# Kernel tuning notes

Hardware: AMD Instinct MI355X
Metric: run time of the kernel (lower is better)

Reference implementation:

```python
import jax, jax.numpy as jnp
import numpy as np
import math

B, S, D, H = 2, 2048, 1024, 16
DK = D // H

def setup_inputs() -> dict:
    key = jax.random.key(0)
    ks = jax.random.split(key, 12)
    scale = 0.02
    return {
        "q": jax.random.normal(ks[0], (B, S, D), jnp.float32),
        "k": jax.random.normal(ks[1], (B, S, D), jnp.float32),
        "v": jax.random.normal(ks[2], (B, S, D), jnp.float32),
        "mask": jnp.ones((B, S), jnp.int32),
        "Wq": jax.random.normal(ks[3], (D, D), jnp.float32) * scale,
        "bq": jnp.zeros((D,), jnp.float32),
        "Wk": jax.random.normal(ks[4], (D, D), jnp.float32) * scale,
        "bk": jnp.zeros((D,), jnp.float32),
        "Wv": jax.random.normal(ks[5], (D, D), jnp.float32) * scale,
        "bv": jnp.zeros((D,), jnp.float32),
        "Wo": jax.random.normal(ks[6], (D, D), jnp.float32) * scale,
        "bo": jnp.zeros((D,), jnp.float32),
    }

def _split_heads(x):
    b, s, d = x.shape
    return x.reshape(b, s, H, DK).transpose(0, 2, 1, 3)  # [b,h,s,dk]

def reference(q, k, v, mask, Wq, bq, Wk, bk, Wv, bv, Wo, bo):
    Q = _split_heads(q @ Wq.T + bq)
    K = _split_heads(k @ Wk.T + bk)
    V = _split_heads(v @ Wv.T + bv)
    scores = jnp.einsum('bhqd,bhkd->bhqk', Q, K) / math.sqrt(DK)
    # mask dim==2 path: [b,s] -> [b,1,1,s]
    m = mask[:, None, None, :]
    scores = jnp.where(m == 0, jnp.float32(-1e9), scores)
    attn = jax.nn.softmax(scores, axis=-1)  # dropout is identity in eval
    out = jnp.einsum('bhqk,bhkd->bhqd', attn, V)
    out = out.transpose(0, 2, 1, 3).reshape(q.shape[0], q.shape[1], D)
    return out @ Wo.T + bo
```

## Files before the change

### kernel.cpp

```cpp
#include <hip/hip_runtime.h>
#include <math.h>

#define D_MODEL 1024
#define NHEAD   16
#define DKH     64
#define SEQ     2048
#define BATCH   2
#define TOK     (BATCH*SEQ)

typedef short s16x8 __attribute__((ext_vector_type(8)));
typedef float f32x4 __attribute__((ext_vector_type(4)));
typedef unsigned short ushort_t;

__device__ inline unsigned short f2bf(float f) {
    union { float f; unsigned u; } v; v.f = f;
    unsigned r = v.u + 0x7FFFu + ((v.u >> 16) & 1u);
    return (unsigned short)(r >> 16);
}
__device__ inline float bf2f(ushort_t h) {
    union { unsigned u; float f; } v; v.u = (unsigned)h << 16;
    return v.f;
}
__device__ inline unsigned cvt_pk_bf16(float a, float b) {
    unsigned r;
    asm("v_cvt_pk_bf16_f32 %0, %1, %2" : "=v"(r) : "v"(a), "v"(b));
    return r;
}
__device__ inline void gload16(const void* g, void* l) {
    __builtin_amdgcn_global_load_lds(
        (const __attribute__((address_space(1))) void*)g,
        (__attribute__((address_space(3))) void*)l, 16, 0, 0);
}

__global__ __launch_bounds__(256) void convert_all(
    const float* __restrict__ q, const float* __restrict__ k,
    const float* __restrict__ v,
    const float* __restrict__ Wq, const float* __restrict__ Wk,
    const float* __restrict__ Wv, const float* __restrict__ Wo,
    const int* __restrict__ mask,
    ushort_t* __restrict__ qb, ushort_t* __restrict__ kb,
    ushort_t* __restrict__ vb,
    ushort_t* __restrict__ Wqb, ushort_t* __restrict__ Wkb,
    ushort_t* __restrict__ Wvb, ushort_t* __restrict__ Wohi,
    ushort_t* __restrict__ Wolo, float* __restrict__ mb)
{
    const int ACT4 = TOK * D_MODEL / 4;
    const int W4   = D_MODEL * D_MODEL / 4;
    const int total = 3 * ACT4 + 4 * W4 + TOK / 4;
    for (int u = blockIdx.x * 256 + threadIdx.x; u < total; u += gridDim.x * 256) {
        if (u < 3 * ACT4) {
            int which = u / ACT4, off = u - which * ACT4;
            const float* src = which == 0 ? q : which == 1 ? k : v;
            ushort_t*    dst = which == 0 ? qb : which == 1 ? kb : vb;
            float4 f = ((const float4*)src)[off];
            uint2 o;
            o.x = cvt_pk_bf16(f.x, f.y);
            o.y = cvt_pk_bf16(f.z, f.w);
            ((uint2*)dst)[off] = o;
        } else if (u < 3 * ACT4 + 3 * W4) {
            int uu = u - 3 * ACT4;
            int which = uu / W4, off = uu - which * W4;
            const float* src = which == 0 ? Wq : which == 1 ? Wk : Wv;
            ushort_t*    dst = which == 0 ? Wqb : which == 1 ? Wkb : Wvb;
            float4 f = ((const float4*)src)[off];
            uint2 o;
            o.x = cvt_pk_bf16(f.x, f.y);
            o.y = cvt_pk_bf16(f.z, f.w);
            ((uint2*)dst)[off] = o;
        } else if (u < 3 * ACT4 + 4 * W4) {
            int off = u - (3 * ACT4 + 3 * W4);
            float4 f = ((const float4*)Wo)[off];
            ushort_t h0 = f2bf(f.x), h1 = f2bf(f.y), h2 = f2bf(f.z), h3 = f2bf(f.w);
            uint2 hw;
            hw.x = (unsigned)h0 | ((unsigned)h1 << 16);
            hw.y = (unsigned)h2 | ((unsigned)h3 << 16);
            ((uint2*)Wohi)[off] = hw;
            uint2 lw;
            lw.x = cvt_pk_bf16(f.x - bf2f(h0), f.y - bf2f(h1));
            lw.y = cvt_pk_bf16(f.z - bf2f(h2), f.w - bf2f(h3));
            ((uint2*)Wolo)[off] = lw;
        } else {
            int off = u - (3 * ACT4 + 4 * W4);
            int4 m = ((const int4*)mask)[off];
            float4 f;
            f.x = m.x ? 0.f : -1e9f;
            f.y = m.y ? 0.f : -1e9f;
            f.z = m.z ? 0.f : -1e9f;
            f.w = m.w ? 0.f : -1e9f;
            ((float4*)mb)[off] = f;
        }
    }
}

__global__ __launch_bounds__(256) void gemm_qkv(
    const ushort_t* __restrict__ qb, const ushort_t* __restrict__ kb,
    const ushort_t* __restrict__ vb,
    const ushort_t* __restrict__ Wqb, const ushort_t* __restrict__ Wkb,
    const ushort_t* __restrict__ Wvb,
    const float* __restrict__ bqp, const float* __restrict__ bkp,
    const float* __restrict__ bvp,
    ushort_t* __restrict__ Qb, ushort_t* __restrict__ Kb,
    ushort_t* __restrict__ Vtb)
{
    __shared__ __align__(16) char pool[64 * 136 * 2];
    ushort_t* As = (ushort_t*)pool;
    ushort_t* Ws = As + 128 * 32;

    const int z = blockIdx.z;
    const ushort_t* Ain  = z == 0 ? qb : z == 1 ? kb : vb;
    const ushort_t* Wptr = z == 0 ? Wqb : z == 1 ? Wkb : Wvb;
    const float*    bias = z == 0 ? bqp : z == 1 ? bkp : bvp;

    const int hwid = blockIdx.x + 8 * blockIdx.y;
    const int work = (hwid & 7) * 32 + (hwid >> 3);
    const int m0 = (work >> 3) * 128;
    const int n0 = (work & 7) * 128;

    const int t = threadIdx.x;
    const int w = t >> 6, lane = t & 63, l15 = lane & 15, l4 = lane >> 4;
    const int wr = w >> 1, wc = w & 1;

    f32x4 acc[4][4];
#pragma unroll
    for (int m = 0; m < 4; ++m)
#pragma unroll
        for (int n = 0; n < 4; ++n) acc[m][n] = (f32x4){0.f, 0.f, 0.f, 0.f};

    const ushort_t* Ag = Ain  + (size_t)(m0 + (t >> 2)) * D_MODEL + (t & 3) * 8;
    const ushort_t* Wg = Wptr + (size_t)(n0 + (t >> 2)) * D_MODEL + (t & 3) * 8;
    ushort_t* AsW = As + w * 512;
    ushort_t* WsW = Ws + w * 512;

    for (int k0 = 0; k0 < D_MODEL; k0 += 32) {
        __syncthreads();
        gload16(Ag + k0, AsW);
        gload16(Ag + (size_t)64 * D_MODEL + k0, AsW + 2048);
        gload16(Wg + k0, WsW);
        gload16(Wg + (size_t)64 * D_MODEL + k0, WsW + 2048);
        __syncthreads();

        s16x8 af[4], bfr[4];
#pragma unroll
        for (int m = 0; m < 4; ++m)
            af[m] = *(const s16x8*)&As[(wr * 64 + m * 16 + l15) * 32 + l4 * 8];
#pragma unroll
        for (int n = 0; n < 4; ++n)
            bfr[n] = *(const s16x8*)&Ws[(wc * 64 + n * 16 + l15) * 32 + l4 * 8];
#pragma unroll
        for (int m = 0; m < 4; ++m)
#pragma unroll
            for (int n = 0; n < 4; ++n)
                acc[m][n] = __builtin_amdgcn_mfma_f32_16x16x32_bf16(af[m], bfr[n], acc[m][n], 0, 0, 0);
    }

    if (z == 2) {
        ushort_t* Ct = (ushort_t*)pool;
        const int h0 = n0 >> 6;
        const int bb = m0 >> 11;
        const int s0 = m0 & (SEQ - 1);
#pragma unroll
        for (int hh = 0; hh < 2; ++hh) {
            __syncthreads();
            if (wc == hh) {
#pragma unroll
                for (int n = 0; n < 4; ++n) {
                    const int nl = n * 16 + l15;
                    const float bv = bias[n0 + hh * 64 + nl];
#pragma unroll
                    for (int m = 0; m < 4; ++m) {
                        const int ml = wr * 64 + m * 16 + l4 * 4;
#pragma unroll
                        for (int r = 0; r < 4; ++r)
                            Ct[nl * 136 + ml + r] = f2bf(acc[m][n][r] + bv);
                    }
                }
            }
            __syncthreads();
            const int dl = t >> 2;
            ushort_t* dst = Vtb + (((size_t)bb * NHEAD + h0 + hh) * DKH + dl) * SEQ + s0;
#pragma unroll
            for (int c = 0; c < 4; ++c) {
                int chk = (t & 3) + c * 4;
                *(uint4*)&dst[chk * 8] = *(const uint4*)&Ct[dl * 136 + chk * 8];
            }
        }
    } else {
        ushort_t* Cout = z == 0 ? Qb : Kb;
#pragma unroll
        for (int n = 0; n < 4; ++n) {
            const int col = n0 + wc * 64 + n * 16 + l15;
            const float bv = bias[col];
#pragma unroll
            for (int m = 0; m < 4; ++m) {
                const int row = m0 + wr * 64 + m * 16 + l4 * 4;
#pragma unroll
                for (int r = 0; r < 4; ++r)
                    Cout[(size_t)(row + r) * D_MODEL + col] = f2bf(acc[m][n][r] + bv);
            }
        }
    }
}

__global__ __launch_bounds__(256) void gemm_out(
    const ushort_t* __restrict__ Ain, const ushort_t* __restrict__ Wptr,
    const ushort_t* __restrict__ W2ptr, const float* __restrict__ bias,
    float* __restrict__ Cout)
{
    __shared__ ushort_t As[128 * 32];
    __shared__ ushort_t Ws[64 * 32];
    __shared__ ushort_t Ws2[64 * 32];

    const int hwid = blockIdx.x + 16 * blockIdx.y;
    const int work = (hwid & 7) * 64 + (hwid >> 3);
    const int m0 = (work >> 4) * 128;
    const int n0 = (work & 15) * 64;

    const int t = threadIdx.x;
    const int w = t >> 6, lane = t & 63, l15 = lane & 15, l4 = lane >> 4;
    const int wr = w >> 1, wc = w & 1;

    f32x4 acc[4][2];
#pragma unroll
    for (int m = 0; m < 4; ++m)
#pragma unroll
        for (int n = 0; n < 2; ++n) acc[m][n] = (f32x4){0.f, 0.f, 0.f, 0.f};

    const ushort_t* Ag  = Ain   + (size_t)(m0 + (t >> 2)) * D_MODEL + (t & 3) * 8;
    const ushort_t* Wg  = Wptr  + (size_t)(n0 + (t >> 2)) * D_MODEL + (t & 3) * 8;
    const ushort_t* W2g = W2ptr + (size_t)(n0 + (t >> 2)) * D_MODEL + (t & 3) * 8;
    ushort_t* AsW = As + w * 512;
    ushort_t* WsW = Ws + w * 512;
    ushort_t* Ws2W = Ws2 + w * 512;

    for (int k0 = 0; k0 < D_MODEL; k0 += 32) {
        __syncthreads();
        gload16(Ag + k0, AsW);
        gload16(Ag + (size_t)64 * D_MODEL + k0, AsW + 2048);
        gload16(Wg + k0, WsW);
        gload16(W2g + k0, Ws2W);
        __syncthreads();

        s16x8 af[4], bfr[2], bfr2[2];
#pragma unroll
        for (int m = 0; m < 4; ++m)
            af[m] = *(const s16x8*)&As[(wr * 64 + m * 16 + l15) * 32 + l4 * 8];
#pragma unroll
        for (int n = 0; n < 2; ++n) {
            bfr[n]  = *(const s16x8*)&Ws[(wc * 32 + n * 16 + l15) * 32 + l4 * 8];
            bfr2[n] = *(const s16x8*)&Ws2[(wc * 32 + n * 16 + l15) * 32 + l4 * 8];
        }
#pragma unroll
        for (int m = 0; m < 4; ++m)
#pragma unroll
            for (int n = 0; n < 2; ++n) {
                acc[m][n] = __builtin_amdgcn_mfma_f32_16x16x32_bf16(af[m], bfr[n],  acc[m][n], 0, 0, 0);
                acc[m][n] = __builtin_amdgcn_mfma_f32_16x16x32_bf16(af[m], bfr2[n], acc[m][n], 0, 0, 0);
            }
    }

#pragma unroll
    for (int n = 0; n < 2; ++n) {
        const int col = n0 + wc * 32 + n * 16 + l15;
        const float bv = bias[col];
#pragma unroll
        for (int m = 0; m < 4; ++m) {
            const int row = m0 + wr * 64 + m * 16 + l4 * 4;
#pragma unroll
            for (int r = 0; r < 4; ++r)
                Cout[(size_t)(row + r) * D_MODEL + col] = acc[m][n][r] + bv;
        }
    }
}

__global__ __launch_bounds__(256) void flash2(
    const ushort_t* __restrict__ Q, const ushort_t* __restrict__ K,
    const ushort_t* __restrict__ Vt, const float* __restrict__ mb,
    ushort_t* __restrict__ Ctx)
{
    __shared__ ushort_t Ks[64 * 72];
    __shared__ ushort_t Vs[64 * 72];
    __shared__ ushort_t Ps[64 * 72];

    const int t = threadIdx.x;
    const int w = t >> 6, lane = t & 63, l15 = lane & 15, l4 = lane >> 4;
    const int q0 = blockIdx.y * 64;
    const int bh = blockIdx.x, b = bh >> 4, h = bh & 15;

    s16x8 qf0, qf1;
    {
        const ushort_t* qp = Q + ((size_t)b * SEQ + q0 + w * 16 + l15) * D_MODEL + h * DKH + l4 * 8;
        qf0 = *(const s16x8*)qp;
        qf1 = *(const s16x8*)(qp + 32);
    }

    f32x4 oacc[4];
#pragma unroll
    for (int dt = 0; dt < 4; ++dt) oacc[dt] = (f32x4){0.f, 0.f, 0.f, 0.f};
    float lpart[4] = {0.f, 0.f, 0.f, 0.f};

    const int ch   = t & 7;
    const int row0 = t >> 3;
    const ushort_t* Kg = K  + ((size_t)b * SEQ) * D_MODEL + h * DKH + ch * 8;
    const ushort_t* Vg = Vt + ((size_t)bh * DKH) * SEQ + ch * 8;

    uint4 kr0 = *(const uint4*)&Kg[(size_t)row0 * D_MODEL];
    uint4 kr1 = *(const uint4*)&Kg[(size_t)(row0 + 32) * D_MODEL];
    uint4 vr0 = *(const uint4*)&Vg[(size_t)row0 * SEQ];
    uint4 vr1 = *(const uint4*)&Vg[(size_t)(row0 + 32) * SEQ];

    const float CSC = 0.18033688011112042f;
    const float* mbp = mb + b * SEQ;

    for (int k0 = 0; k0 < SEQ; k0 += 64) {
        __syncthreads();
        *(uint4*)&Ks[row0 * 72 + ch * 8]        = kr0;
        *(uint4*)&Ks[(row0 + 32) * 72 + ch * 8] = kr1;
        *(uint4*)&Vs[row0 * 72 + ch * 8]        = vr0;
        *(uint4*)&Vs[(row0 + 32) * 72 + ch * 8] = vr1;
        __syncthreads();
        if (k0 + 64 < SEQ) {
            kr0 = *(const uint4*)&Kg[(size_t)(k0 + 64 + row0) * D_MODEL];
            kr1 = *(const uint4*)&Kg[(size_t)(k0 + 64 + row0 + 32) * D_MODEL];
            vr0 = *(const uint4*)&Vg[(size_t)row0 * SEQ + k0 + 64];
            vr1 = *(const uint4*)&Vg[(size_t)(row0 + 32) * SEQ + k0 + 64];
        }
        float mbv[4];
#pragma unroll
        for (int ct = 0; ct < 4; ++ct) mbv[ct] = mbp[k0 + ct * 16 + l15];

        f32x4 sacc[4];
#pragma unroll
        for (int ct = 0; ct < 4; ++ct) sacc[ct] = (f32x4){0.f, 0.f, 0.f, 0.f};
        __builtin_amdgcn_s_setprio(1);
#pragma unroll
        for (int ct = 0; ct < 4; ++ct) {
            s16x8 b0 = *(const s16x8*)&Ks[(ct * 16 + l15) * 72 + l4 * 8];
            s16x8 b1 = *(const s16x8*)&Ks[(ct * 16 + l15) * 72 + 32 + l4 * 8];
            sacc[ct] = __builtin_amdgcn_mfma_f32_16x16x32_bf16(qf0, b0, sacc[ct], 0, 0, 0);
            sacc[ct] = __builtin_amdgcn_mfma_f32_16x16x32_bf16(qf1, b1, sacc[ct], 0, 0, 0);
        }
        __builtin_amdgcn_s_setprio(0);

#pragma unroll
        for (int ct = 0; ct < 4; ++ct) {
            float p0 = __builtin_amdgcn_exp2f(fmaf(sacc[ct][0], CSC, mbv[ct]));
            float p1 = __builtin_amdgcn_exp2f(fmaf(sacc[ct][1], CSC, mbv[ct]));
            float p2 = __builtin_amdgcn_exp2f(fmaf(sacc[ct][2], CSC, mbv[ct]));
            float p3 = __builtin_amdgcn_exp2f(fmaf(sacc[ct][3], CSC, mbv[ct]));
            lpart[0] += p0; lpart[1] += p1; lpart[2] += p2; lpart[3] += p3;
            unsigned u01 = cvt_pk_bf16(p0, p1);
            unsigned u23 = cvt_pk_bf16(p2, p3);
            int base = (w * 16 + l4 * 4) * 72 + ct * 16 + l15;
            Ps[base]       = (ushort_t)u01;
            Ps[base + 72]  = (ushort_t)(u01 >> 16);
            Ps[base + 144] = (ushort_t)u23;
            Ps[base + 216] = (ushort_t)(u23 >> 16);
        }

        __builtin_amdgcn_s_setprio(1);
#pragma unroll
        for (int ks = 0; ks < 2; ++ks) {
            s16x8 af = *(const s16x8*)&Ps[(w * 16 + l15) * 72 + ks * 32 + l4 * 8];
#pragma unroll
            for (int dt = 0; dt < 4; ++dt) {
                s16x8 bf = *(const s16x8*)&Vs[(dt * 16 + l15) * 72 + ks * 32 + l4 * 8];
                oacc[dt] = __builtin_amdgcn_mfma_f32_16x16x32_bf16(af, bf, oacc[dt], 0, 0, 0);
            }
        }
        __builtin_amdgcn_s_setprio(0);
    }

#pragma unroll
    for (int r = 0; r < 4; ++r) {
        lpart[r] += __shfl_xor(lpart[r], 1);
        lpart[r] += __shfl_xor(lpart[r], 2);
        lpart[r] += __shfl_xor(lpart[r], 4);
        lpart[r] += __shfl_xor(lpart[r], 8);
    }
    const size_t obase = ((size_t)b * SEQ + q0 + w * 16 + l4 * 4) * D_MODEL + h * DKH + l15;
#pragma unroll
    for (int r = 0; r < 4; ++r) {
        float inv = 1.f / lpart[r];
#pragma unroll
        for (int dt = 0; dt < 4; ++dt)
            Ctx[obase + (size_t)r * D_MODEL + dt * 16] = f2bf(oacc[dt][r] * inv);
    }
}

extern "C" void kernel_launch(void* const* d_in, const int* in_sizes, int n_in,
                              void* d_out, int out_size, void* d_ws, size_t ws_size,
                              hipStream_t stream) {
    const float* q    = (const float*)d_in[0];
    const float* k    = (const float*)d_in[1];
    const float* v    = (const float*)d_in[2];
    const int*   mask = (const int*)  d_in[3];
    const float* Wq   = (const float*)d_in[4];
    const float* bq   = (const float*)d_in[5];
    const float* Wk   = (const float*)d_in[6];
    const float* bk   = (const float*)d_in[7];
    const float* Wv   = (const float*)d_in[8];
    const float* bv   = (const float*)d_in[9];
    const float* Wo   = (const float*)d_in[10];
    const float* bo   = (const float*)d_in[11];
    float* out = (float*)d_out;

    char* ws = (char*)d_ws;
    ushort_t* Wqb  = (ushort_t*)(ws);
    ushort_t* Wkb  = (ushort_t*)(ws + ( 2u << 20));
    ushort_t* Wvb  = (ushort_t*)(ws + ( 4u << 20));
    ushort_t* Wohi = (ushort_t*)(ws + ( 6u << 20));
    ushort_t* Wolo = (ushort_t*)(ws + ( 8u << 20));
    float*    mb   = (float*)   (ws + (10u << 20));
    ushort_t* qb   = (ushort_t*)(ws + (12u << 20));
    ushort_t* kb   = (ushort_t*)(ws + (20u << 20));
    ushort_t* vb   = (ushort_t*)(ws + (28u << 20));
    ushort_t* Qb   = (ushort_t*)(ws + (36u << 20));
    ushort_t* Kb   = (ushort_t*)(ws + (44u << 20));
    ushort_t* Vtb  = (ushort_t*)(ws + (52u << 20));
    ushort_t* Ctx  = qb;

    convert_all<<<2048, 256, 0, stream>>>(q, k, v, Wq, Wk, Wv, Wo, mask,
                                          qb, kb, vb, Wqb, Wkb, Wvb,
                                          Wohi, Wolo, mb);

    dim3 qkvgrid(D_MODEL / 128, TOK / 128, 3);
    gemm_qkv<<<qkvgrid, 256, 0, stream>>>(qb, kb, vb, Wqb, Wkb, Wvb,
                                          bq, bk, bv, Qb, Kb, Vtb);

    dim3 agrid(BATCH * NHEAD, SEQ / 64);
    flash2<<<agrid, 256, 0, stream>>>(Qb, Kb, Vtb, mb, Ctx);

    dim3 ogrid(D_MODEL / 64, TOK / 128);
    gemm_out<<<ogrid, 256, 0, stream>>>(Ctx, Wohi, Wolo, bo, out);
}
```

Before: 156.5 us.

## Switch attention kernel to 32x32x16 MFMA with 128-query tiles per block

The attention kernel now uses 32x32x16 bf16 MFMA instructions instead of 16x16x32, with each wave owning 32 query rows, so a block covers 128 queries instead of 64. This halves the number of blocks and doubles the reuse of each K/V tile loaded into shared memory. It also changes the fragment layouts for P staging and the row-sum reduction. The trade-offs are higher register pressure (16-wide accumulators and 16 row partial sums), a larger P buffer in shared memory, and fewer blocks to spread across the GPU.

```diff
diff --git a/kernel.cpp b/kernel.cpp
--- a/kernel.cpp
+++ b/kernel.cpp
@@ -10,6 +10,7 @@
 
 typedef short s16x8 __attribute__((ext_vector_type(8)));
 typedef float f32x4 __attribute__((ext_vector_type(4)));
+typedef float f32x16 __attribute__((ext_vector_type(16)));
 typedef unsigned short ushort_t;
 
 __device__ inline unsigned short f2bf(float f) {
@@ -30,6 +31,12 @@
     __builtin_amdgcn_global_load_lds(
         (const __attribute__((address_space(1))) void*)g,
         (__attribute__((address_space(3))) void*)l, 16, 0, 0);
+}
+__device__ inline f32x16 zero16() {
+    f32x16 v;
+#pragma unroll
+    for (int i = 0; i < 16; ++i) v[i] = 0.f;
+    return v;
 }
 
 __global__ __launch_bounds__(256) void convert_all(
@@ -272,31 +279,33 @@
     }
 }
 
-__global__ __launch_bounds__(256) void flash2(
+__global__ __launch_bounds__(256) void flash5(
     const ushort_t* __restrict__ Q, const ushort_t* __restrict__ K,
     const ushort_t* __restrict__ Vt, const float* __restrict__ mb,
     ushort_t* __restrict__ Ctx)
 {
     __shared__ ushort_t Ks[64 * 72];
     __shared__ ushort_t Vs[64 * 72];
-    __shared__ ushort_t Ps[64 * 72];
+    __shared__ ushort_t Ps[128 * 72];
 
     const int t = threadIdx.x;
-    const int w = t >> 6, lane = t & 63, l15 = lane & 15, l4 = lane >> 4;
-    const int q0 = blockIdx.y * 64;
+    const int w = t >> 6, lane = t & 63;
+    const int l31 = lane & 31, lh = lane >> 5;
+    const int q0 = blockIdx.y * 128;
     const int bh = blockIdx.x, b = bh >> 4, h = bh & 15;
 
-    s16x8 qf0, qf1;
+    s16x8 qf[4];
     {
-        const ushort_t* qp = Q + ((size_t)b * SEQ + q0 + w * 16 + l15) * D_MODEL + h * DKH + l4 * 8;
-        qf0 = *(const s16x8*)qp;
-        qf1 = *(const s16x8*)(qp + 32);
-    }
-
-    f32x4 oacc[4];
-#pragma unroll
-    for (int dt = 0; dt < 4; ++dt) oacc[dt] = (f32x4){0.f, 0.f, 0.f, 0.f};
-    float lpart[4] = {0.f, 0.f, 0.f, 0.f};
+        const ushort_t* qp = Q + ((size_t)b * SEQ + q0 + w * 32 + l31) * D_MODEL + h * DKH + lh * 8;
+#pragma unroll
+        for (int ks = 0; ks < 4; ++ks)
+            qf[ks] = *(const s16x8*)(qp + ks * 16);
+    }
+
+    f32x16 oacc0 = zero16(), oacc1 = zero16();
+    float lpart[16];
+#pragma unroll
+    for (int i = 0; i < 16; ++i) lpart[i] = 0.f;
 
     const int ch   = t & 7;
     const int row0 = t >> 3;
@@ -310,6 +319,7 @@
 
     const float CSC = 0.18033688011112042f;
     const float* mbp = mb + b * SEQ;
+    const int prow = w * 32;
 
     for (int k0 = 0; k0 < SEQ; k0 += 64) {
         __syncthreads();
@@ -324,66 +334,67 @@
             vr0 = *(const uint4*)&Vg[(size_t)row0 * SEQ + k0 + 64];
             vr1 = *(const uint4*)&Vg[(size_t)(row0 + 32) * SEQ + k0 + 64];
         }
-        float mbv[4];
-#pragma unroll
-        for (int ct = 0; ct < 4; ++ct) mbv[ct] = mbp[k0 + ct * 16 + l15];
-
-        f32x4 sacc[4];
-#pragma unroll
-        for (int ct = 0; ct < 4; ++ct) sacc[ct] = (f32x4){0.f, 0.f, 0.f, 0.f};
+        const float mb0 = mbp[k0 + l31];
+        const float mb1 = mbp[k0 + 32 + l31];
+
+        f32x16 sacc0 = zero16(), sacc1 = zero16();
         __builtin_amdgcn_s_setprio(1);
 #pragma unroll
-        for (int ct = 0; ct < 4; ++ct) {
-            s16x8 b0 = *(const s16x8*)&Ks[(ct * 16 + l15) * 72 + l4 * 8];
-            s16x8 b1 = *(const s16x8*)&Ks[(ct * 16 + l15) * 72 + 32 + l4 * 8];
-            sacc[ct] = __builtin_amdgcn_mfma_f32_16x16x32_bf16(qf0, b0, sacc[ct], 0, 0, 0);
-            sacc[ct] = __builtin_amdgcn_mfma_f32_16x16x32_bf16(qf1, b1, sacc[ct], 0, 0, 0);
+        for (int ks = 0; ks < 4; ++ks) {
+            s16x8 kf0 = *(const s16x8*)&Ks[(l31)      * 72 + ks * 16 + lh * 8];
+            s16x8 kf1 = *(const s16x8*)&Ks[(32 + l31) * 72 + ks * 16 + lh * 8];
+            sacc0 = __builtin_amdgcn_mfma_f32_32x32x16_bf16(qf[ks], kf0, sacc0, 0, 0, 0);
+            sacc1 = __builtin_amdgcn_mfma_f32_32x32x16_bf16(qf[ks], kf1, sacc1, 0, 0, 0);
         }
         __builtin_amdgcn_s_setprio(0);
 
 #pragma unroll
-        for (int ct = 0; ct < 4; ++ct) {
-            float p0 = __builtin_amdgcn_exp2f(fmaf(sacc[ct][0], CSC, mbv[ct]));
-            float p1 = __builtin_amdgcn_exp2f(fmaf(sacc[ct][1], CSC, mbv[ct]));
-            float p2 = __builtin_amdgcn_exp2f(fmaf(sacc[ct][2], CSC, mbv[ct]));
-            float p3 = __builtin_amdgcn_exp2f(fmaf(sacc[ct][3], CSC, mbv[ct]));
-            lpart[0] += p0; lpart[1] += p1; lpart[2] += p2; lpart[3] += p3;
-            unsigned u01 = cvt_pk_bf16(p0, p1);
-            unsigned u23 = cvt_pk_bf16(p2, p3);
-            int base = (w * 16 + l4 * 4) * 72 + ct * 16 + l15;
-            Ps[base]       = (ushort_t)u01;
-            Ps[base + 72]  = (ushort_t)(u01 >> 16);
-            Ps[base + 144] = (ushort_t)u23;
-            Ps[base + 216] = (ushort_t)(u23 >> 16);
-        }
+        for (int rp = 0; rp < 8; ++rp) {
+            const int r0 = 2 * rp;
+            const int rowb = (r0 & 3) + 8 * (r0 >> 2) + 4 * lh;
+            float p0 = __builtin_amdgcn_exp2f(fmaf(sacc0[r0],     CSC, mb0));
+            float p1 = __builtin_amdgcn_exp2f(fmaf(sacc0[r0 + 1], CSC, mb0));
+            float p2 = __builtin_amdgcn_exp2f(fmaf(sacc1[r0],     CSC, mb1));
+            float p3 = __builtin_amdgcn_exp2f(fmaf(sacc1[r0 + 1], CSC, mb1));
+            lpart[r0]     += p0 + p2;
+            lpart[r0 + 1] += p1 + p3;
+            unsigned ua = cvt_pk_bf16(p0, p1);
+            unsigned ub = cvt_pk_bf16(p2, p3);
+            int base0 = (prow + rowb) * 72 + l31;
+            Ps[base0]           = (ushort_t)ua;
+            Ps[base0 + 72]      = (ushort_t)(ua >> 16);
+            Ps[base0 + 32]      = (ushort_t)ub;
+            Ps[base0 + 72 + 32] = (ushort_t)(ub >> 16);
+        }
+        __builtin_amdgcn_sched_barrier(0);
 
         __builtin_amdgcn_s_setprio(1);
 #pragma unroll
-        for (int ks = 0; ks < 2; ++ks) {
-            s16x8 af = *(const s16x8*)&Ps[(w * 16 + l15) * 72 + ks * 32 + l4 * 8];
-#pragma unroll
-            for (int dt = 0; dt < 4; ++dt) {
-                s16x8 bf = *(const s16x8*)&Vs[(dt * 16 + l15) * 72 + ks * 32 + l4 * 8];
-                oacc[dt] = __builtin_amdgcn_mfma_f32_16x16x32_bf16(af, bf, oacc[dt], 0, 0, 0);
-            }
+        for (int ks = 0; ks < 4; ++ks) {
+            s16x8 pa  = *(const s16x8*)&Ps[(prow + l31) * 72 + ks * 16 + lh * 8];
+            s16x8 vf0 = *(const s16x8*)&Vs[(l31)      * 72 + ks * 16 + lh * 8];
+            s16x8 vf1 = *(const s16x8*)&Vs[(32 + l31) * 72 + ks * 16 + lh * 8];
+            oacc0 = __builtin_amdgcn_mfma_f32_32x32x16_bf16(pa, vf0, oacc0, 0, 0, 0);
+            oacc1 = __builtin_amdgcn_mfma_f32_32x32x16_bf16(pa, vf1, oacc1, 0, 0, 0);
         }
         __builtin_amdgcn_s_setprio(0);
     }
 
 #pragma unroll
-    for (int r = 0; r < 4; ++r) {
-        lpart[r] += __shfl_xor(lpart[r], 1);
-        lpart[r] += __shfl_xor(lpart[r], 2);
-        lpart[r] += __shfl_xor(lpart[r], 4);
-        lpart[r] += __shfl_xor(lpart[r], 8);
-    }
-    const size_t obase = ((size_t)b * SEQ + q0 + w * 16 + l4 * 4) * D_MODEL + h * DKH + l15;
-#pragma unroll
-    for (int r = 0; r < 4; ++r) {
-        float inv = 1.f / lpart[r];
-#pragma unroll
-        for (int dt = 0; dt < 4; ++dt)
-            Ctx[obase + (size_t)r * D_MODEL + dt * 16] = f2bf(oacc[dt][r] * inv);
+    for (int rg = 0; rg < 16; ++rg) {
+        lpart[rg] += __shfl_xor(lpart[rg], 1);
+        lpart[rg] += __shfl_xor(lpart[rg], 2);
+        lpart[rg] += __shfl_xor(lpart[rg], 4);
+        lpart[rg] += __shfl_xor(lpart[rg], 8);
+        lpart[rg] += __shfl_xor(lpart[rg], 16);
+    }
+    const size_t obase = ((size_t)b * SEQ + q0 + w * 32) * D_MODEL + h * DKH + l31;
+#pragma unroll
+    for (int rg = 0; rg < 16; ++rg) {
+        const int qrow = (rg & 3) + 8 * (rg >> 2) + 4 * lh;
+        const float inv = 1.f / lpart[rg];
+        Ctx[obase + (size_t)qrow * D_MODEL]      = f2bf(oacc0[rg] * inv);
+        Ctx[obase + (size_t)qrow * D_MODEL + 32] = f2bf(oacc1[rg] * inv);
     }
 }
 
@@ -427,8 +438,8 @@
     gemm_qkv<<<qkvgrid, 256, 0, stream>>>(qb, kb, vb, Wqb, Wkb, Wvb,
                                           bq, bk, bv, Qb, Kb, Vtb);
 
-    dim3 agrid(BATCH * NHEAD, SEQ / 64);
-    flash2<<<agrid, 256, 0, stream>>>(Qb, Kb, Vtb, mb, Ctx);
+    dim3 agrid(BATCH * NHEAD, SEQ / 128);
+    flash5<<<agrid, 256, 0, stream>>>(Qb, Kb, Vtb, mb, Ctx);
 
     dim3 ogrid(D_MODEL / 64, TOK / 128);
     gemm_out<<<ogrid, 256, 0, stream>>>(Ctx, Wohi, Wolo, bo, out);
```

Measured after the change: 150.6 us. 3.8% less time.
